# Optimization experiments

Hardware: AMD Instinct MI355X
Metric: run time of the kernel (lower is better)

The kernel has to match this reference:

```python
import jax, jax.numpy as jnp
import numpy as np

N = 100000      # nodes
E = 3200000     # edges (avg degree 32)
DIN, DH, DOUT = 256, 256, 64
K = 10          # propagation hops


def _uniform(key, shape, fan_in):
    b = 1.0 / np.sqrt(fan_in)
    return jax.random.uniform(key, shape, jnp.float32, -b, b)


def setup_inputs() -> dict:
    key = jax.random.key(0)
    ks = jax.random.split(key, 8)
    x = jax.random.normal(ks[0], (N, DIN), jnp.float32)
    edge_index = jax.random.randint(ks[1], (2, E), 0, N, dtype=jnp.int64)
    W1 = _uniform(ks[2], (DIN, DH), DIN)
    b1 = _uniform(ks[3], (DH,), DIN)
    W2 = _uniform(ks[4], (DH, DOUT), DH)
    b2 = _uniform(ks[5], (DOUT,), DH)
    proj_w = _uniform(ks[6], (DOUT,), DOUT)
    proj_b = _uniform(ks[7], (), DOUT)
    return {"x": x, "edge_index": edge_index, "W1": W1, "b1": b1,
            "W2": W2, "b2": b2, "proj_w": proj_w, "proj_b": proj_b}


def _gcn_norm(edge_index, num_nodes):
    # add self-loops with weight 1, symmetric normalization deg^-1/2 A deg^-1/2
    loops = jnp.arange(num_nodes, dtype=edge_index.dtype)
    row = jnp.concatenate([edge_index[0], loops])
    col = jnp.concatenate([edge_index[1], loops])
    w = jnp.ones(row.shape[0], jnp.float32)
    deg = jax.ops.segment_sum(w, col, num_segments=num_nodes)
    dinv = jnp.where(deg > 0, jax.lax.rsqrt(deg), 0.0)
    norm = dinv[row] * dinv[col]  # edge weight is 1
    return row, col, norm


def reference(x, edge_index, W1, b1, W2, b2, proj_w, proj_b):
    h = jax.nn.relu(x @ W1 + b1)
    h = h @ W2 + b2                               # [N, DOUT]
    row, col, norm = _gcn_norm(edge_index, N)
    preds = [h]
    for _ in range(K):
        h = jax.ops.segment_sum(norm[:, None] * h[row], col, num_segments=N)
        preds.append(h)
    pps = jnp.stack(preds, axis=1)                # [N, K+1, DOUT]
    score = jax.nn.sigmoid(pps @ proj_w + proj_b) # [N, K+1]
    out = jnp.einsum('nk,nkc->nc', score, pps)    # adaptive hop pooling
    return out
```

## Files before the change

### kernel.cpp

```cpp
#include <hip/hip_runtime.h>
#include <hip/hip_bf16.h>
#include <math.h>


#define WAVE 64
#define NBLK 1024

__device__ inline float bf2f(unsigned short u) {
    union { unsigned int i; float f; } v; v.i = ((unsigned int)u) << 16; return v.f;
}
__device__ inline unsigned short f2bf(float f) {
    __hip_bfloat16 b = __float2bfloat16(f);
    union { __hip_bfloat16 b; unsigned short u; } v; v.b = b; return v.u;
}

typedef __attribute__((ext_vector_type(8))) short bf16x8;
typedef __attribute__((ext_vector_type(16))) float f32x16;

__global__ void detect_kernel(const unsigned* __restrict__ e, int* __restrict__ sflag) {
    __shared__ int any;
    if (threadIdx.x == 0) any = 0;
    __syncthreads();
    unsigned nz = 0;
    int t = threadIdx.x;
    for (int i = 0; i < 8; ++i) nz |= e[(size_t)(t * 8 + i) * 2 + 1];
    if (nz) atomicOr(&any, 1);
    __syncthreads();
    if (t == 0) *sflag = any ? 1 : 2;
}

__global__ void passA_kernel(const int* __restrict__ eidx, const int* __restrict__ sflag,
                             int* __restrict__ blk_cnt, int E, int NB, int EPB) {
    __shared__ int lh[512];
    int t = threadIdx.x, blk = blockIdx.x;
    for (int i = t; i < NB; i += 256) lh[i] = 0;
    __syncthreads();
    int s = *sflag;
    int base = blk * EPB;
    int end = base + EPB; if (end > E) end = E;
    for (int e = base + t; e < end; e += 256) {
        int c = eidx[(size_t)s * (size_t)(E + e)];
        atomicAdd(&lh[c >> 8], 1);
    }
    __syncthreads();
    for (int i = t; i < NB; i += 256)
        blk_cnt[(size_t)i * NBLK + blk] = lh[i];
}

__global__ void scan1_kernel(const int* __restrict__ in, int* __restrict__ out,
                             int* __restrict__ bsums, int n) {
    __shared__ int s[256];
    int t = threadIdx.x;
    int idx = blockIdx.x * 1024 + t * 4;
    int x0 = (idx + 0 < n) ? in[idx + 0] : 0;
    int x1 = (idx + 1 < n) ? in[idx + 1] : 0;
    int x2 = (idx + 2 < n) ? in[idx + 2] : 0;
    int x3 = (idx + 3 < n) ? in[idx + 3] : 0;
    int lsum = x0 + x1 + x2 + x3;
    s[t] = lsum;
    __syncthreads();
    for (int o = 1; o < 256; o <<= 1) {
        int v = (t >= o) ? s[t - o] : 0;
        __syncthreads();
        if (t >= o) s[t] += v;
        __syncthreads();
    }
    int excl = s[t] - lsum;
    if (idx + 0 < n) out[idx + 0] = excl;
    if (idx + 1 < n) out[idx + 1] = excl + x0;
    if (idx + 2 < n) out[idx + 2] = excl + x0 + x1;
    if (idx + 3 < n) out[idx + 3] = excl + x0 + x1 + x2;
    if (t == 255) bsums[blockIdx.x] = s[255];
}

__global__ void scan2g_kernel(int* __restrict__ bsums, int nb) {
    __shared__ int part[256];
    int t = threadIdx.x;
    int v[4]; int run = 0;
    #pragma unroll
    for (int j = 0; j < 4; ++j) {
        int i = t * 4 + j;
        int x = (i < nb) ? bsums[i] : 0;
        v[j] = run; run += x;
    }
    part[t] = run;
    __syncthreads();
    for (int o = 1; o < 256; o <<= 1) {
        int x = (t >= o) ? part[t - o] : 0;
        __syncthreads();
        if (t >= o) part[t] += x;
        __syncthreads();
    }
    int excl = part[t] - run;
    #pragma unroll
    for (int j = 0; j < 4; ++j) {
        int i = t * 4 + j;
        if (i < nb) bsums[i] = excl + v[j];
    }
}

__global__ void scan3_kernel(int* __restrict__ arr, const int* __restrict__ bsums,
                             int n, int total) {
    int t = threadIdx.x;
    int idx = blockIdx.x * 1024 + t * 4;
    int add = bsums[blockIdx.x];
    #pragma unroll
    for (int i = 0; i < 4; ++i)
        if (idx + i < n) arr[idx + i] += add;
    if (blockIdx.x == 0 && t == 0) arr[n] = total;
}

__global__ void passB_kernel(const int* __restrict__ eidx, const int* __restrict__ sflag,
                             const int* __restrict__ pbase, int2* __restrict__ pairs,
                             int E, int NB, int EPB) {
    __shared__ int lcur[512];
    int t = threadIdx.x, blk = blockIdx.x;
    for (int i = t; i < NB; i += 256) lcur[i] = pbase[(size_t)i * NBLK + blk];
    __syncthreads();
    int s = *sflag;
    int base = blk * EPB;
    int end = base + EPB; if (end > E) end = E;
    for (int e = base + t; e < end; e += 256) {
        int r = eidx[(size_t)s * (size_t)e];
        int c = eidx[(size_t)s * (size_t)(E + e)];
        int pos = atomicAdd(&lcur[c >> 8], 1);
        pairs[pos] = make_int2(r, c);
    }
}

__global__ void passD_kernel(const int2* __restrict__ pairs, const int* __restrict__ pbase,
                             int* __restrict__ cnt, int N) {
    __shared__ int lcnt[256];
    int b = blockIdx.x, t = threadIdx.x;
    lcnt[t] = 0;
    __syncthreads();
    int w0 = pbase[(size_t)b * NBLK], w1 = pbase[(size_t)(b + 1) * NBLK];
    for (int i = w0 + t; i < w1; i += 256)
        atomicAdd(&lcnt[pairs[i].y & 255], 1);
    __syncthreads();
    int node = b * 256 + t;
    if (node < N) cnt[node] = lcnt[t];
}

__global__ void dinv_kernel(const int* __restrict__ cnt, float* __restrict__ dinv, int n) {
    int i = blockIdx.x * blockDim.x + threadIdx.x;
    if (i < n) dinv[i] = rsqrtf((float)(cnt[i] + 1));
}

__global__ void passC_kernel(const int2* __restrict__ pairs, const int* __restrict__ pbase,
                             const int* __restrict__ offs, int* __restrict__ csr_src,
                             int N) {
    __shared__ int lcur[256];
    int b = blockIdx.x, t = threadIdx.x;
    int node = b * 256 + t;
    lcur[t] = (node < N) ? offs[node] : 0;
    __syncthreads();
    int w0 = pbase[(size_t)b * NBLK], w1 = pbase[(size_t)(b + 1) * NBLK];
    for (int i = w0 + t; i < w1; i += 256) {
        int2 p = pairs[i];
        int pos = atomicAdd(&lcur[p.y & 255], 1);
        csr_src[pos] = p.x;
    }
}

__global__ void wconv_kernel(const float* __restrict__ W, unsigned short* __restrict__ Wt,
                             int K, int Nn) {
    int i = blockIdx.x * blockDim.x + threadIdx.x;
    if (i >= K * Nn) return;
    int n = i / K, k = i - n * K;
    Wt[(size_t)n * K + k] = f2bf(W[(size_t)k * Nn + n]);
}

__global__ __launch_bounds__(256, 1) void mlp_fused(
        const float* __restrict__ x,
        const unsigned short* __restrict__ W1t,
        const float* __restrict__ b1,
        const unsigned short* __restrict__ W2t,
        const float* __restrict__ b2,
        const float* __restrict__ dinv,
        const float* __restrict__ pw, const float* __restrict__ pb,
        float* __restrict__ out, unsigned short* __restrict__ g,
        int M) {
    __shared__ unsigned short xfrag[2][2][128 * 8];
    __shared__ unsigned short w1frag[2][2][256 * 8];
    __shared__ unsigned short h1frag[16][2][128 * 8];
    __shared__ unsigned short w2frag[16][2][64 * 8];

    int tid = threadIdx.x;
    int wave = tid >> 6, lane = tid & 63;
    int half = lane >> 5, l31 = lane & 31;
    int wm = wave >> 1, wn = wave & 1;
    int bm = blockIdx.x * 128;

    #pragma unroll
    for (int i = 0; i < 8; ++i) {
        int F = i * 256 + tid;
        int s = F >> 7, hf = (F >> 6) & 1, n = F & 63;
        uint4 u = *(const uint4*)(W2t + (size_t)n * 256 + s * 16 + hf * 8);
        *(uint4*)&w2frag[s][hf][n * 8] = u;
    }

    f32x16 acc1[2][4] = {};

    float4 xv[4];
    uint4 wv[4];
    #pragma unroll
    for (int i = 0; i < 4; ++i) {
        int f = i * 256 + tid;
        int row = f >> 3, c4 = (f & 7) * 4;
        int grow = bm + row;
        xv[i] = (grow < M) ? *(const float4*)(x + (size_t)grow * 256 + c4)
                           : make_float4(0.f, 0.f, 0.f, 0.f);
    }
    {
        const unsigned short* p = W1t + (size_t)tid * 256;
        wv[0] = *(const uint4*)(p);
        wv[1] = *(const uint4*)(p + 8);
        wv[2] = *(const uint4*)(p + 16);
        wv[3] = *(const uint4*)(p + 24);
    }

    for (int it = 0; it < 8; ++it) {
        #pragma unroll
        for (int i = 0; i < 4; ++i) {
            int f = i * 256 + tid;
            int row = f >> 3, c4 = (f & 7) * 4;
            int k16 = c4 >> 4, hf = (c4 >> 3) & 1, off = c4 & 7;
            ushort4 u;
            u.x = f2bf(xv[i].x); u.y = f2bf(xv[i].y);
            u.z = f2bf(xv[i].z); u.w = f2bf(xv[i].w);
            *(ushort4*)&xfrag[k16][hf][row * 8 + off] = u;
        }
        #pragma unroll
        for (int q = 0; q < 4; ++q)
            *(uint4*)&w1frag[q >> 1][q & 1][tid * 8] = wv[q];
        __syncthreads();
        if (it < 7) {
            int k0 = (it + 1) * 32;
            #pragma unroll
            for (int i = 0; i < 4; ++i) {
                int f = i * 256 + tid;
                int row = f >> 3, c4 = (f & 7) * 4;
                int grow = bm + row;
                xv[i] = (grow < M) ? *(const float4*)(x + (size_t)grow * 256 + k0 + c4)
                                   : make_float4(0.f, 0.f, 0.f, 0.f);
            }
            const unsigned short* p = W1t + (size_t)tid * 256 + k0;
            wv[0] = *(const uint4*)(p);
            wv[1] = *(const uint4*)(p + 8);
            wv[2] = *(const uint4*)(p + 16);
            wv[3] = *(const uint4*)(p + 24);
        }
        #pragma unroll
        for (int s = 0; s < 2; ++s) {
            bf16x8 a0 = *(bf16x8*)&xfrag[s][half][(wm * 64 + l31) * 8];
            bf16x8 a1 = *(bf16x8*)&xfrag[s][half][(wm * 64 + 32 + l31) * 8];
            #pragma unroll
            for (int j = 0; j < 4; ++j) {
                bf16x8 b = *(bf16x8*)&w1frag[s][half][(wn * 128 + j * 32 + l31) * 8];
                acc1[0][j] = __builtin_amdgcn_mfma_f32_32x32x16_bf16(a0, b, acc1[0][j], 0, 0, 0);
                acc1[1][j] = __builtin_amdgcn_mfma_f32_32x32x16_bf16(a1, b, acc1[1][j], 0, 0, 0);
            }
        }
        __syncthreads();
    }

    #pragma unroll
    for (int j = 0; j < 4; ++j) {
        int ch = wn * 128 + j * 32 + l31;
        float bb = b1[ch];
        int k16 = ch >> 4, hf = (ch >> 3) & 1, off = ch & 7;
        #pragma unroll
        for (int mt = 0; mt < 2; ++mt) {
            #pragma unroll
            for (int reg = 0; reg < 16; ++reg) {
                int rowin = (reg & 3) + 8 * (reg >> 2) + 4 * half;
                int row = wm * 64 + mt * 32 + rowin;
                float v = fmaxf(acc1[mt][j][reg] + bb, 0.f);
                h1frag[k16][hf][row * 8 + off] = f2bf(v);
            }
        }
    }
    __syncthreads();

    f32x16 acc2[2] = {};
    #pragma unroll
    for (int s = 0; s < 16; ++s) {
        bf16x8 a = *(bf16x8*)&h1frag[s][half][(wave * 32 + l31) * 8];
        #pragma unroll
        for (int j = 0; j < 2; ++j) {
            bf16x8 b = *(bf16x8*)&w2frag[s][half][(j * 32 + l31) * 8];
            acc2[j] = __builtin_amdgcn_mfma_f32_32x32x16_bf16(a, b, acc2[j], 0, 0, 0);
        }
    }

    float bb0 = b2[l31], bb1 = b2[32 + l31];
    float pw0 = pw[l31], pw1 = pw[32 + l31];
    float pbv = pb[0];
    #pragma unroll
    for (int reg = 0; reg < 16; ++reg) {
        int rowin = (reg & 3) + 8 * (reg >> 2) + 4 * half;
        int row = bm + wave * 32 + rowin;
        float h0 = acc2[0][reg] + bb0;
        float h1v = acc2[1][reg] + bb1;
        float d = h0 * pw0 + h1v * pw1;
        d += __shfl_xor(d, 1, 64);
        d += __shfl_xor(d, 2, 64);
        d += __shfl_xor(d, 4, 64);
        d += __shfl_xor(d, 8, 64);
        d += __shfl_xor(d, 16, 64);
        float sg = 1.f / (1.f + __expf(-(d + pbv)));
        if (row < M) {
            float dv = dinv[row];
            out[(size_t)row * 64 + l31]      = sg * h0;
            out[(size_t)row * 64 + 32 + l31] = sg * h1v;
            g[(size_t)row * 64 + l31]        = f2bf(dv * h0);
            g[(size_t)row * 64 + 32 + l31]   = f2bf(dv * h1v);
        }
    }
}

__global__ void spmm_kernel(const int* __restrict__ offs, const int* __restrict__ src,
                            const float* __restrict__ dinv,
                            const __hip_bfloat16* __restrict__ gin,
                            __hip_bfloat16* __restrict__ gout,
                            float* __restrict__ out,
                            const float* __restrict__ pw, const float* __restrict__ pb,
                            int n) {
    int wid = (blockIdx.x * blockDim.x + threadIdx.x) >> 6;
    int lane = threadIdx.x & 63;
    if (wid >= n) return;
    int c = __builtin_amdgcn_readfirstlane(wid);
    int e = __builtin_amdgcn_readfirstlane(offs[c]);
    int eend = __builtin_amdgcn_readfirstlane(offs[c + 1]);
    float acc = 0.f;
    while (e < eend && (e & 3)) {
        acc += __bfloat162float(gin[(size_t)src[e] * 64 + lane]);
        ++e;
    }
    for (; e + 7 < eend; e += 8) {
        int4 sa = *(const int4*)(src + e);
        int4 sb = *(const int4*)(src + e + 4);
        float v0 = __bfloat162float(gin[(size_t)sa.x * 64 + lane]);
        float v1 = __bfloat162float(gin[(size_t)sa.y * 64 + lane]);
        float v2 = __bfloat162float(gin[(size_t)sa.z * 64 + lane]);
        float v3 = __bfloat162float(gin[(size_t)sa.w * 64 + lane]);
        float v4 = __bfloat162float(gin[(size_t)sb.x * 64 + lane]);
        float v5 = __bfloat162float(gin[(size_t)sb.y * 64 + lane]);
        float v6 = __bfloat162float(gin[(size_t)sb.z * 64 + lane]);
        float v7 = __bfloat162float(gin[(size_t)sb.w * 64 + lane]);
        acc += ((v0 + v1) + (v2 + v3)) + ((v4 + v5) + (v6 + v7));
    }
    for (; e + 3 < eend; e += 4) {
        int4 sa = *(const int4*)(src + e);
        float v0 = __bfloat162float(gin[(size_t)sa.x * 64 + lane]);
        float v1 = __bfloat162float(gin[(size_t)sa.y * 64 + lane]);
        float v2 = __bfloat162float(gin[(size_t)sa.z * 64 + lane]);
        float v3 = __bfloat162float(gin[(size_t)sa.w * 64 + lane]);
        acc += (v0 + v1) + (v2 + v3);
    }
    for (; e < eend; ++e) acc += __bfloat162float(gin[(size_t)src[e] * 64 + lane]);

    float dc = dinv[c];
    float h = dc * (acc + __bfloat162float(gin[(size_t)c * 64 + lane]));
    gout[(size_t)c * 64 + lane] = __float2bfloat16(dc * h);
    float d = h * pw[lane];
    #pragma unroll
    for (int o = 32; o > 0; o >>= 1) d += __shfl_xor(d, o, 64);
    float sg = 1.f / (1.f + __expf(-(d + pb[0])));
    out[(size_t)c * 64 + lane] += sg * h;
}

extern "C" void kernel_launch(void* const* d_in, const int* in_sizes, int n_in,
                              void* d_out, int out_size, void* d_ws, size_t ws_size,
                              hipStream_t stream) {
    const float* x  = (const float*)d_in[0];
    const int* eidx = (const int*)d_in[1];
    const float* W1 = (const float*)d_in[2];
    const float* b1 = (const float*)d_in[3];
    const float* W2 = (const float*)d_in[4];
    const float* b2 = (const float*)d_in[5];
    const float* pw = (const float*)d_in[6];
    const float* pb = (const float*)d_in[7];
    float* out = (float*)d_out;

    const int N = in_sizes[0] / 256;
    const int E = in_sizes[1] / 2;
    const int NB = (N + 255) >> 8;
    const int EPB = (E + NBLK - 1) / NBLK;
    const int M = NB * NBLK;

    size_t woff = 0;
    auto alloc = [&](size_t bytes) -> void* {
        void* p = (char*)d_ws + woff;
        woff += (bytes + 255) & ~(size_t)255;
        return p;
    };
    int*   sflag   = (int*)alloc(4);
    int*   cnt     = (int*)alloc((size_t)N * 4);
    float* dinv    = (float*)alloc((size_t)N * 4);
    int*   offs    = (int*)alloc(((size_t)N + 1) * 4);
    int*   bsums   = (int*)alloc(1024 * 4);
    int*   bsums2  = (int*)alloc(1024 * 4);
    int*   pbase   = (int*)alloc(((size_t)M + 1) * 4);
    int*   csr_src = (int*)alloc((size_t)E * 4);
    int2*  pairs   = (int2*)alloc((size_t)E * 8);
    unsigned short* W1t = (unsigned short*)alloc((size_t)256 * 256 * 2);
    unsigned short* W2t = (unsigned short*)alloc((size_t)64 * 256 * 2);
    __hip_bfloat16* gA = (__hip_bfloat16*)alloc((size_t)N * 64 * 2);
    __hip_bfloat16* gB = (__hip_bfloat16*)alloc((size_t)N * 64 * 2);

    detect_kernel<<<1, 256, 0, stream>>>((const unsigned*)eidx, sflag);

    passA_kernel<<<NBLK, 256, 0, stream>>>(eidx, sflag, pbase, E, NB, EPB);
    int nb2 = (M + 1023) / 1024;
    scan1_kernel<<<nb2, 256, 0, stream>>>(pbase, pbase, bsums2, M);
    scan2g_kernel<<<1, 256, 0, stream>>>(bsums2, nb2);
    scan3_kernel<<<nb2, 256, 0, stream>>>(pbase, bsums2, M, E);
    passB_kernel<<<NBLK, 256, 0, stream>>>(eidx, sflag, pbase, pairs, E, NB, EPB);
    passD_kernel<<<NB, 256, 0, stream>>>(pairs, pbase, cnt, N);
    dinv_kernel<<<(N + 255) / 256, 256, 0, stream>>>(cnt, dinv, N);
    int nb1 = (N + 1023) / 1024;
    scan1_kernel<<<nb1, 256, 0, stream>>>(cnt, offs, bsums, N);
    scan2g_kernel<<<1, 256, 0, stream>>>(bsums, nb1);
    scan3_kernel<<<nb1, 256, 0, stream>>>(offs, bsums, N, E);
    passC_kernel<<<NB, 256, 0, stream>>>(pairs, pbase, offs, csr_src, N);

    wconv_kernel<<<(256 * 256 + 255) / 256, 256, 0, stream>>>(W1, W1t, 256, 256);
    wconv_kernel<<<(64 * 256 + 255) / 256, 256, 0, stream>>>(W2, W2t, 256, 64);
    int gb = (N + 127) / 128;
    mlp_fused<<<gb, 256, 0, stream>>>(x, W1t, b1, W2t, b2, dinv, pw, pb,
                                      out, (unsigned short*)gA, N);

    int nwb = (N + 3) / 4;
    __hip_bfloat16* gin = gA;
    __hip_bfloat16* gout = gB;
    for (int k = 0; k < 10; ++k) {
        spmm_kernel<<<nwb, 256, 0, stream>>>(offs, csr_src, dinv, gin, gout, out, pw, pb, N);
        __hip_bfloat16* t = gin; gin = gout; gout = t;
    }
}
```

Before: 1.150 ms.

## Shrink MLP tile to 64 rows, read weights from global, raise occupancy

```diff
diff --git a/kernel.cpp b/kernel.cpp
--- a/kernel.cpp
+++ b/kernel.cpp
@@ -5,6 +5,7 @@
 
 #define WAVE 64
 #define NBLK 1024
+#define RS 520
 
 __device__ inline float bf2f(unsigned short u) {
     union { unsigned int i; float f; } v; v.i = ((unsigned int)u) << 16; return v.f;
@@ -171,7 +172,7 @@
     Wt[(size_t)n * K + k] = f2bf(W[(size_t)k * Nn + n]);
 }
 
-__global__ __launch_bounds__(256, 1) void mlp_fused(
+__global__ __launch_bounds__(256, 4) void mlp_fused(
         const float* __restrict__ x,
         const unsigned short* __restrict__ W1t,
         const float* __restrict__ b1,
@@ -181,85 +182,60 @@
         const float* __restrict__ pw, const float* __restrict__ pb,
         float* __restrict__ out, unsigned short* __restrict__ g,
         int M) {
-    __shared__ unsigned short xfrag[2][2][128 * 8];
-    __shared__ unsigned short w1frag[2][2][256 * 8];
-    __shared__ unsigned short h1frag[16][2][128 * 8];
-    __shared__ unsigned short w2frag[16][2][64 * 8];
+    __shared__ unsigned short xfrag[4 * RS];
+    __shared__ unsigned short h1frag[32 * RS];
 
     int tid = threadIdx.x;
     int wave = tid >> 6, lane = tid & 63;
     int half = lane >> 5, l31 = lane & 31;
-    int wm = wave >> 1, wn = wave & 1;
-    int bm = blockIdx.x * 128;
-
-    #pragma unroll
-    for (int i = 0; i < 8; ++i) {
-        int F = i * 256 + tid;
-        int s = F >> 7, hf = (F >> 6) & 1, n = F & 63;
-        uint4 u = *(const uint4*)(W2t + (size_t)n * 256 + s * 16 + hf * 8);
-        *(uint4*)&w2frag[s][hf][n * 8] = u;
-    }
-
-    f32x16 acc1[2][4] = {};
-
-    float4 xv[4];
-    uint4 wv[4];
-    #pragma unroll
-    for (int i = 0; i < 4; ++i) {
+    int rt = wave & 1;
+    int cw = wave >> 1;
+    int bm = blockIdx.x * 64;
+
+    f32x16 acc1[4] = {};
+
+    float4 xv[2];
+    #pragma unroll
+    for (int i = 0; i < 2; ++i) {
         int f = i * 256 + tid;
         int row = f >> 3, c4 = (f & 7) * 4;
         int grow = bm + row;
         xv[i] = (grow < M) ? *(const float4*)(x + (size_t)grow * 256 + c4)
                            : make_float4(0.f, 0.f, 0.f, 0.f);
     }
-    {
-        const unsigned short* p = W1t + (size_t)tid * 256;
-        wv[0] = *(const uint4*)(p);
-        wv[1] = *(const uint4*)(p + 8);
-        wv[2] = *(const uint4*)(p + 16);
-        wv[3] = *(const uint4*)(p + 24);
-    }
 
     for (int it = 0; it < 8; ++it) {
         #pragma unroll
-        for (int i = 0; i < 4; ++i) {
+        for (int i = 0; i < 2; ++i) {
             int f = i * 256 + tid;
             int row = f >> 3, c4 = (f & 7) * 4;
-            int k16 = c4 >> 4, hf = (c4 >> 3) & 1, off = c4 & 7;
+            int region = c4 >> 3, off = c4 & 7;
             ushort4 u;
             u.x = f2bf(xv[i].x); u.y = f2bf(xv[i].y);
             u.z = f2bf(xv[i].z); u.w = f2bf(xv[i].w);
-            *(ushort4*)&xfrag[k16][hf][row * 8 + off] = u;
-        }
-        #pragma unroll
-        for (int q = 0; q < 4; ++q)
-            *(uint4*)&w1frag[q >> 1][q & 1][tid * 8] = wv[q];
+            *(ushort4*)&xfrag[region * RS + row * 8 + off] = u;
+        }
         __syncthreads();
         if (it < 7) {
             int k0 = (it + 1) * 32;
             #pragma unroll
-            for (int i = 0; i < 4; ++i) {
+            for (int i = 0; i < 2; ++i) {
                 int f = i * 256 + tid;
                 int row = f >> 3, c4 = (f & 7) * 4;
                 int grow = bm + row;
                 xv[i] = (grow < M) ? *(const float4*)(x + (size_t)grow * 256 + k0 + c4)
                                    : make_float4(0.f, 0.f, 0.f, 0.f);
             }
-            const unsigned short* p = W1t + (size_t)tid * 256 + k0;
-            wv[0] = *(const uint4*)(p);
-            wv[1] = *(const uint4*)(p + 8);
-            wv[2] = *(const uint4*)(p + 16);
-            wv[3] = *(const uint4*)(p + 24);
-        }
+        }
+        int kg = it * 32 + half * 8;
         #pragma unroll
         for (int s = 0; s < 2; ++s) {
-            bf16x8 a0 = *(bf16x8*)&xfrag[s][half][(wm * 64 + l31) * 8];
-            bf16x8 a1 = *(bf16x8*)&xfrag[s][half][(wm * 64 + 32 + l31) * 8];
+            bf16x8 a = *(bf16x8*)&xfrag[(s * 2 + half) * RS + (rt * 32 + l31) * 8];
             #pragma unroll
             for (int j = 0; j < 4; ++j) {
-                bf16x8 b = *(bf16x8*)&w1frag[s][half][(wn * 128 + j * 32 + l31) * 8];
-                acc1[0][j] = __builtin_amdgcn_mfma_f32_32x32x16_bf16(a0, b, acc1[0][j], 0, 0, 0);
-                acc1[1][j] = __builtin_amdgcn_mfma_f32_32x32x16_bf16(a1, b, acc1[1][j], 0, 0, 0);
+                int ch = cw * 128 + j * 32 + l31;
+                bf16x8 b = *(const bf16x8*)(W1t + (size_t)ch * 256 + kg + s * 16);
+                acc1[j] = __builtin_amdgcn_mfma_f32_32x32x16_bf16(a, b, acc1[j], 0, 0, 0);
             }
         }
         __syncthreads();
@@ -267,55 +243,53 @@
 
     #pragma unroll
     for (int j = 0; j < 4; ++j) {
-        int ch = wn * 128 + j * 32 + l31;
+        int ch = cw * 128 + j * 32 + l31;
         float bb = b1[ch];
-        int k16 = ch >> 4, hf = (ch >> 3) & 1, off = ch & 7;
+        int region = ch >> 3, off = ch & 7;
         #pragma unroll
-        for (int mt = 0; mt < 2; ++mt) {
+        for (int reg = 0; reg < 16; ++reg) {
+            int rowin = (reg & 3) + 8 * (reg >> 2) + 4 * half;
+            int row = rt * 32 + rowin;
+            float v = fmaxf(acc1[j][reg] + bb, 0.f);
+            h1frag[region * RS + row * 8 + off] = f2bf(v);
+        }
+    }
+    __syncthreads();
+
+    if (wave < 2) {
+        f32x16 acc2[2] = {};
+        #pragma unroll
+        for (int s = 0; s < 16; ++s) {
+            bf16x8 a = *(bf16x8*)&h1frag[(s * 2 + half) * RS + (wave * 32 + l31) * 8];
             #pragma unroll
-            for (int reg = 0; reg < 16; ++reg) {
-                int rowin = (reg & 3) + 8 * (reg >> 2) + 4 * half;
-                int row = wm * 64 + mt * 32 + rowin;
-                float v = fmaxf(acc1[mt][j][reg] + bb, 0.f);
-                h1frag[k16][hf][row * 8 + off] = f2bf(v);
+            for (int j = 0; j < 2; ++j) {
+                bf16x8 b = *(const bf16x8*)(W2t + (size_t)(j * 32 + l31) * 256 + s * 16 + half * 8);
+                acc2[j] = __builtin_amdgcn_mfma_f32_32x32x16_bf16(a, b, acc2[j], 0, 0, 0);
             }
         }
-    }
-    __syncthreads();
-
-    f32x16 acc2[2] = {};
-    #pragma unroll
-    for (int s = 0; s < 16; ++s) {
-        bf16x8 a = *(bf16x8*)&h1frag[s][half][(wave * 32 + l31) * 8];
+        float bb0 = b2[l31], bb1 = b2[32 + l31];
+        float pw0 = pw[l31], pw1 = pw[32 + l31];
+        float pbv = pb[0];
         #pragma unroll
-        for (int j = 0; j < 2; ++j) {
-            bf16x8 b = *(bf16x8*)&w2frag[s][half][(j * 32 + l31) * 8];
-            acc2[j] = __builtin_amdgcn_mfma_f32_32x32x16_bf16(a, b, acc2[j], 0, 0, 0);
-        }
-    }
-
-    float bb0 = b2[l31], bb1 = b2[32 + l31];
-    float pw0 = pw[l31], pw1 = pw[32 + l31];
-    float pbv = pb[0];
-    #pragma unroll
-    for (int reg = 0; reg < 16; ++reg) {
-        int rowin = (reg & 3) + 8 * (reg >> 2) + 4 * half;
-        int row = bm + wave * 32 + rowin;
-        float h0 = acc2[0][reg] + bb0;
-        float h1v = acc2[1][reg] + bb1;
-        float d = h0 * pw0 + h1v * pw1;
-        d += __shfl_xor(d, 1, 64);
-        d += __shfl_xor(d, 2, 64);
-        d += __shfl_xor(d, 4, 64);
-        d += __shfl_xor(d, 8, 64);
-        d += __shfl_xor(d, 16, 64);
-        float sg = 1.f / (1.f + __expf(-(d + pbv)));
-        if (row < M) {
-            float dv = dinv[row];
-            out[(size_t)row * 64 + l31]      = sg * h0;
-            out[(size_t)row * 64 + 32 + l31] = sg * h1v;
-            g[(size_t)row * 64 + l31]        = f2bf(dv * h0);
-            g[(size_t)row * 64 + 32 + l31]   = f2bf(dv * h1v);
+        for (int reg = 0; reg < 16; ++reg) {
+            int rowin = (reg & 3) + 8 * (reg >> 2) + 4 * half;
+            int row = bm + wave * 32 + rowin;
+            float h0 = acc2[0][reg] + bb0;
+            float h1v = acc2[1][reg] + bb1;
+            float d = h0 * pw0 + h1v * pw1;
+            d += __shfl_xor(d, 1, 64);
+            d += __shfl_xor(d, 2, 64);
+            d += __shfl_xor(d, 4, 64);
+            d += __shfl_xor(d, 8, 64);
+            d += __shfl_xor(d, 16, 64);
+            float sg = 1.f / (1.f + __expf(-(d + pbv)));
+            if (row < M) {
+                float dv = dinv[row];
+                out[(size_t)row * 64 + l31]      = sg * h0;
+                out[(size_t)row * 64 + 32 + l31] = sg * h1v;
+                g[(size_t)row * 64 + l31]        = f2bf(dv * h0);
+                g[(size_t)row * 64 + 32 + l31]   = f2bf(dv * h1v);
+            }
         }
     }
 }
@@ -428,7 +402,7 @@
 
     wconv_kernel<<<(256 * 256 + 255) / 256, 256, 0, stream>>>(W1, W1t, 256, 256);
     wconv_kernel<<<(64 * 256 + 255) / 256, 256, 0, stream>>>(W2, W2t, 256, 64);
-    int gb = (N + 127) / 128;
+    int gb = (N + 63) / 64;
     mlp_fused<<<gb, 256, 0, stream>>>(x, W1t, b1, W2t, b2, dinv, pw, pb,
                                       out, (unsigned short*)gA, N);
 
```

New measurement: 1.112 ms. -3.3%, faster.
